# Performance work log

Hardware: AMD Instinct MI355X
Metric: run time of the kernel (lower is better)

Reference implementation:

```python
import jax, jax.numpy as jnp
import numpy as np

B, T, U = 32, 4096, 512

def setup_inputs() -> dict:
    key = jax.random.key(0)
    k1, k2 = jax.random.split(key)
    x = jax.random.normal(k1, (B, T, U), dtype=jnp.float32)
    # learned per-channel smoothing coefficient (Keras 'uniform' init)
    b = jax.random.uniform(k2, (U,), dtype=jnp.float32)
    return {"x": x, "b": b}

def reference(x, b):
    # EMA recurrence: y_t = b * x_t + (1 - b) * y_{t-1}, y_0 state = 0.
    # First-order linear recurrence y_t = a * y_{t-1} + c_t solved with a
    # parallel (log-depth) associative scan over the time axis.
    a = 1.0 - b                      # (U,) decay per channel
    c = b * x                        # (B, T, U) input injection
    A = jnp.broadcast_to(a, c.shape) # (B, T, U)

    def combine(left, right):
        a_l, c_l = left
        a_r, c_r = right
        return (a_l * a_r, a_r * c_l + c_r)

    _, y = jax.lax.associative_scan(combine, (A, c), axis=1)
    return y  # (B, T, U) full output sequence
```

## Files before the change

kernel.cpp:

```cpp
#include <hip/hip_runtime.h>
#include <hip/hip_fp16.h>


namespace {

typedef float f4 __attribute__((ext_vector_type(4)));

constexpr int kB  = 32;
constexpr int kT  = 4096;
constexpr int kU4 = 512 / 4;
constexpr int kC  = 64;
constexpr int kL  = kT / kC;

constexpr size_t kSBytes  = (size_t)kB * kC * kU4 * sizeof(f4);
constexpr size_t kYlBytes = (size_t)kB * kT * kU4 * 8;
constexpr size_t kWsNeedStash = kSBytes + kYlBytes;
constexpr size_t kWsNeedBasic = kSBytes;

__device__ __forceinline__ f4 fma4(f4 a, f4 b, f4 c) {
  f4 r;
  r.x = fmaf(a.x, b.x, c.x);
  r.y = fmaf(a.y, b.y, c.y);
  r.z = fmaf(a.z, b.z, c.z);
  r.w = fmaf(a.w, b.w, c.w);
  return r;
}

union PkH4 { uint2 u; __half2 h[2]; };


__global__ __launch_bounds__(256) void ema_s1(
    const float* __restrict__ x, const float* __restrict__ bc,
    f4* __restrict__ S, uint2* __restrict__ yl) {
  const int bid  = blockIdx.x;
  const int b    = bid >> 5;
  const int pair = bid & 31;
  const int sub  = threadIdx.x >> 7;
  const int u4   = threadIdx.x & 127;
  const int k    = pair * 2 + sub;

  const f4 bb = ((const f4*)bc)[u4];
  const f4 a  = 1.0f - bb;

  const size_t off = ((size_t)b * kT + (size_t)k * kL) * kU4 + u4;
  const f4* xp = (const f4*)x + off;
  uint2*    yp = yl + off;

  f4 s = (f4)0.f;
  #pragma unroll 8
  for (int t = 0; t < kL; ++t) {
    f4 v = __builtin_nontemporal_load(xp + (size_t)t * kU4);
    s = fma4(a, s, bb * v);
    PkH4 pk;
    pk.h[0] = __floats2half2_rn(s.x, s.y);
    pk.h[1] = __floats2half2_rn(s.z, s.w);
    yp[(size_t)t * kU4] = pk.u;
  }
  S[((size_t)b * kC + k) * kU4 + u4] = s;
}

__global__ __launch_bounds__(256) void ema_s2(
    const float* __restrict__ bc, const f4* __restrict__ S,
    const uint2* __restrict__ yl, float* __restrict__ out) {
  const int bid  = blockIdx.x;
  const int b    = bid >> 5;
  const int pair = bid & 31;
  const int sub  = threadIdx.x >> 7;
  const int u4   = threadIdx.x & 127;
  const int k    = pair * 2 + sub;

  const f4 bb = ((const f4*)bc)[u4];
  const f4 a  = 1.0f - bb;
  f4 a64 = a;
  #pragma unroll
  for (int j = 0; j < 6; ++j) a64 *= a64;

  f4 e = (f4)0.f;
  f4 w = (f4)1.f;
  const f4* Sp = S + (size_t)b * kC * kU4 + u4;
  #pragma unroll 4
  for (int j = k - 1; j >= 0; --j) {
    e = fma4(w, Sp[(size_t)j * kU4], e);
    w *= a64;
  }

  const size_t off = ((size_t)b * kT + (size_t)k * kL) * kU4 + u4;
  const uint2* yp = yl + off;
  f4*          op = (f4*)out + off;
  f4 p = a;
  #pragma unroll 8
  for (int t = 0; t < kL; ++t) {
    PkH4 pk;
    pk.u = yp[(size_t)t * kU4];
    float2 lo = __half22float2(pk.h[0]);
    float2 hi = __half22float2(pk.h[1]);
    f4 yv;
    yv.x = fmaf(p.x, e.x, lo.x);
    yv.y = fmaf(p.y, e.y, lo.y);
    yv.z = fmaf(p.z, e.z, hi.x);
    yv.w = fmaf(p.w, e.w, hi.y);
    __builtin_nontemporal_store(yv, op + (size_t)t * kU4);
    p *= a;
  }
}


__global__ __launch_bounds__(256) void ema_p1(
    const float* __restrict__ x, const float* __restrict__ bc,
    f4* __restrict__ S) {
  const int bid  = blockIdx.x;
  const int b    = bid >> 5;
  const int pair = bid & 31;
  const int sub  = threadIdx.x >> 7;
  const int u4   = threadIdx.x & 127;
  const int k    = pair * 2 + sub;

  const f4 bb = ((const f4*)bc)[u4];
  const f4 a  = 1.0f - bb;

  const f4* xp = (const f4*)x + ((size_t)b * kT + (size_t)k * kL) * kU4 + u4;
  f4 s = (f4)0.f;
  #pragma unroll 8
  for (int t = 0; t < kL; ++t) s = fma4(a, s, bb * xp[(size_t)t * kU4]);
  S[((size_t)b * kC + k) * kU4 + u4] = s;
}

__global__ __launch_bounds__(256) void ema_p23(
    const float* __restrict__ x, const float* __restrict__ bc,
    const f4* __restrict__ S, float* __restrict__ out) {
  const int bid  = blockIdx.x;
  const int b    = bid >> 5;
  const int pair = bid & 31;
  const int sub  = threadIdx.x >> 7;
  const int u4   = threadIdx.x & 127;
  const int k    = pair * 2 + sub;

  const f4 bb = ((const f4*)bc)[u4];
  const f4 a  = 1.0f - bb;
  f4 a64 = a;
  #pragma unroll
  for (int j = 0; j < 6; ++j) a64 *= a64;

  f4 e = (f4)0.f;
  f4 w = (f4)1.f;
  const f4* Sp = S + (size_t)b * kC * kU4 + u4;
  #pragma unroll 4
  for (int j = k - 1; j >= 0; --j) {
    e = fma4(w, Sp[(size_t)j * kU4], e);
    w *= a64;
  }

  const size_t off = ((size_t)b * kT + (size_t)k * kL) * kU4 + u4;
  const f4* xp = (const f4*)x + off;
  f4*       op = (f4*)out + off;
  f4 y = e;
  #pragma unroll 8
  for (int t = 0; t < kL; ++t) {
    y = fma4(a, y, bb * xp[(size_t)t * kU4]);
    __builtin_nontemporal_store(y, op + (size_t)t * kU4);
  }
}


__global__ __launch_bounds__(256) void ema_fallback(
    const float* __restrict__ x, const float* __restrict__ bc,
    float* __restrict__ out) {
  int g = blockIdx.x * 256 + threadIdx.x;
  if (g >= kB * kU4) return;
  int u4 = g % kU4;
  int b  = g / kU4;
  const f4 bb = ((const f4*)bc)[u4];
  const f4 a  = 1.0f - bb;
  f4 y = (f4)0.f;
  size_t off = (size_t)b * kT * kU4 + u4;
  const f4* xp = (const f4*)x + off;
  f4*       op = (f4*)out + off;
  for (int t = 0; t < kT; ++t) {
    y = fma4(a, y, bb * xp[(size_t)t * kU4]);
    op[(size_t)t * kU4] = y;
  }
}

}

extern "C" void kernel_launch(void* const* d_in, const int* in_sizes, int n_in,
                              void* d_out, int out_size, void* d_ws, size_t ws_size,
                              hipStream_t stream) {
  const float* x  = (const float*)d_in[0];
  const float* bc = (const float*)d_in[1];
  float* out = (float*)d_out;
  const int grid = kB * (kC / 2);

  if (ws_size >= kWsNeedStash) {
    f4*    S  = (f4*)d_ws;
    uint2* yl = (uint2*)((char*)d_ws + kSBytes);
    ema_s1<<<grid, 256, 0, stream>>>(x, bc, S, yl);
    ema_s2<<<grid, 256, 0, stream>>>(bc, S, yl, out);
  } else if (ws_size >= kWsNeedBasic) {
    f4* S = (f4*)d_ws;
    ema_p1 <<<grid, 256, 0, stream>>>(x, bc, S);
    ema_p23<<<grid, 256, 0, stream>>>(x, bc, S, out);
  } else {
    ema_fallback<<<(kB * kU4 + 255) / 256, 256, 0, stream>>>(x, bc, out);
  }
}
```

Measured before the change: 136.8 us.

## Add single-pass cooperative EMA kernel with decoupled lookback via global flags

Adds a cooperative kernel that reads x once into registers and computes per-chunk partial states. It publishes those states to global memory with release flags, spins until every chunk in the same batch and quarter is ready, then scans the published states to get its carry-in and writes the output. This removes the second pass over x, or the fp16 stash round trip, of the earlier two-kernel schemes. The cost is an extra flag-zeroing launch, a cooperative launch, and spin-wait synchronisation across four sequential quarters. Chunks also scan all 32 partial states redundantly.

After: 523.9 us. 283% more time.

```diff
diff --git a/kernel.cpp b/kernel.cpp
--- a/kernel.cpp
+++ b/kernel.cpp
@@ -9,9 +9,19 @@
 constexpr int kB  = 32;
 constexpr int kT  = 4096;
 constexpr int kU4 = 512 / 4;
+
+constexpr int kQ  = 4;
+constexpr int kKQ = 32;
+constexpr int kCL = 32;
+constexpr int kHL = 16;
+
+constexpr size_t kFlagCount = (size_t)kQ * kB * 64;
+constexpr size_t kSOff      = 32768;
+constexpr size_t kSElemsC   = (size_t)kQ * kB * kKQ * kU4;
+constexpr size_t kWsCoop    = kSOff + kSElemsC * sizeof(f4);
+
 constexpr int kC  = 64;
 constexpr int kL  = kT / kC;
-
 constexpr size_t kSBytes  = (size_t)kB * kC * kU4 * sizeof(f4);
 constexpr size_t kYlBytes = (size_t)kB * kT * kU4 * 8;
 constexpr size_t kWsNeedStash = kSBytes + kYlBytes;
@@ -27,6 +37,91 @@
 }
 
 union PkH4 { uint2 u; __half2 h[2]; };
+
+
+__global__ __launch_bounds__(256) void ema_zeroflags(unsigned* f) {
+  int i = blockIdx.x * 256 + threadIdx.x;
+  if (i < (int)kFlagCount) f[i] = 0u;
+}
+
+__global__ __launch_bounds__(256, 4) void ema_coop(
+    const float* __restrict__ x, const float* __restrict__ bc,
+    f4* __restrict__ S, unsigned* __restrict__ flags,
+    float* __restrict__ out) {
+  const int bid  = blockIdx.x;
+  const int b    = bid >> 5;
+  const int k    = bid & 31;
+  const int u4   = threadIdx.x & 127;
+  const int half = threadIdx.x >> 7;
+  const int lane = threadIdx.x & 63;
+  const int wv   = threadIdx.x >> 6;
+
+  __shared__ f4 lds_s0[kU4];
+  __shared__ f4 lds_e[kU4];
+
+  const f4 bb = ((const f4*)bc)[u4];
+  const f4 a  = 1.0f - bb;
+  f4 a16 = a;
+  #pragma unroll
+  for (int j = 0; j < 4; ++j) a16 *= a16;
+  const f4 a32 = a16 * a16;
+
+  f4 seed = (f4)0.f;
+
+  for (int q = 0; q < kQ; ++q) {
+    const size_t base =
+        ((size_t)b * kT + (size_t)q * (kKQ * kCL) + (size_t)k * kCL +
+         (size_t)half * kHL) * kU4 + u4;
+    const f4* xp = (const f4*)x + base;
+    f4 xv[kHL];
+    #pragma unroll
+    for (int i = 0; i < kHL; ++i) xv[i] = xp[(size_t)i * kU4];
+    f4 s = (f4)0.f;
+    #pragma unroll
+    for (int i = 0; i < kHL; ++i) s = fma4(a, s, bb * xv[i]);
+
+    if (half == 0) lds_s0[u4] = s;
+    __syncthreads();
+
+    unsigned* fl = flags + ((size_t)q * kB + b) * 64;
+    f4*       Sq = S + ((size_t)q * kB + b) * (kKQ * kU4);
+
+    if (half == 1) {
+      const f4 Sk = fma4(a16, lds_s0[u4], s);
+      Sq[(size_t)k * kU4 + u4] = Sk;
+      if (lane == 0)
+        __hip_atomic_store(fl + (k * 2 + (wv - 2)), 1u,
+                           __ATOMIC_RELEASE, __HIP_MEMORY_SCOPE_AGENT);
+      for (;;) {
+        unsigned f = __hip_atomic_load(fl + lane, __ATOMIC_RELAXED,
+                                       __HIP_MEMORY_SCOPE_AGENT);
+        if (__all(f == 1u)) break;
+        __builtin_amdgcn_s_sleep(1);
+      }
+      __builtin_amdgcn_fence(__ATOMIC_ACQUIRE, "agent");
+      f4 efull = seed, ek = seed;
+      const f4* Sp = Sq + u4;
+      #pragma unroll 8
+      for (int j = 0; j < kKQ; ++j) {
+        if (j == k) ek = efull;
+        efull = fma4(a32, efull, Sp[(size_t)j * kU4]);
+      }
+      seed = efull;
+      lds_e[u4] = ek;
+    }
+    __syncthreads();
+
+    const f4 E = lds_e[u4];
+    f4 y = (half == 0) ? E : fma4(a16, E, lds_s0[u4]);
+    f4* op = (f4*)out + base;
+    #pragma unroll
+    for (int i = 0; i < kHL; ++i) {
+      y = fma4(a, y, bb * xv[i]);
+      op[(size_t)i * kU4] = y;
+    }
+    __syncthreads();
+  }
+}
 
 
 __global__ __launch_bounds__(256) void ema_s1(
@@ -162,7 +257,7 @@
 }
 
 
-__global__ __launch_bounds__(256) void ema_fallback(
+__global__ __launch_bounds__(256) void ema_seq(
     const float* __restrict__ x, const float* __restrict__ bc,
     float* __restrict__ out) {
   int g = blockIdx.x * 256 + threadIdx.x;
@@ -190,6 +285,17 @@
   const float* bc = (const float*)d_in[1];
   float* out = (float*)d_out;
   const int grid = kB * (kC / 2);
+
+  if (ws_size >= kWsCoop) {
+    unsigned* flags = (unsigned*)d_ws;
+    f4*       S     = (f4*)((char*)d_ws + kSOff);
+    ema_zeroflags<<<(int)((kFlagCount + 255) / 256), 256, 0, stream>>>(flags);
+    void* args[] = {(void*)&x, (void*)&bc, (void*)&S, (void*)&flags,
+                    (void*)&out};
+    hipError_t err = hipLaunchCooperativeKernel(
+        (const void*)ema_coop, dim3(kB * kKQ), dim3(256), args, 0, stream);
+    if (err == hipSuccess) return;
+  }
 
   if (ws_size >= kWsNeedStash) {
     f4*    S  = (f4*)d_ws;
@@ -201,6 +307,6 @@
     ema_p1 <<<grid, 256, 0, stream>>>(x, bc, S);
     ema_p23<<<grid, 256, 0, stream>>>(x, bc, S, out);
   } else {
-    ema_fallback<<<(kB * kU4 + 255) / 256, 256, 0, stream>>>(x, bc, out);
-  }
-}
+    ema_seq<<<(kB * kU4 + 255) / 256, 256, 0, stream>>>(x, bc, out);
+  }
+}
```
